# Performance work log

Hardware: AMD Instinct MI355X
Metric: run time of the kernel (lower is better)

Reference implementation:

```python
import jax, jax.numpy as jnp
import numpy as np

N_NODES = 50000
N_EDGES = 800000
DIM = 128
N_LAYERS = 4
EPS = 1e-5  # BatchNorm1d default eps


def setup_inputs() -> dict:
    key = jax.random.key(0)
    k_x, k_e, k_w = jax.random.split(key, 3)
    x = jax.random.normal(k_x, (N_NODES, DIM), dtype=jnp.float32)
    edge_index = jax.random.randint(k_e, (2, N_EDGES), 0, N_NODES, dtype=jnp.int32)
    # stacked per-layer params (input_dim == hidden_dim == DIM)
    Ws = jax.random.normal(k_w, (N_LAYERS, DIM, DIM), dtype=jnp.float32) * (1.0 / np.sqrt(DIM))
    bs = jnp.zeros((N_LAYERS, DIM), jnp.float32)
    gammas = jnp.ones((N_LAYERS, DIM), jnp.float32)
    betas = jnp.zeros((N_LAYERS, DIM), jnp.float32)
    return {"x": x, "edge_index": edge_index, "Ws": Ws, "bs": bs,
            "gammas": gammas, "betas": betas}


def gcn_conv(x, W, b, src, dst, n):
    # PyG GCNConv: h = X W; out = D^{-1/2}(A+I)D^{-1/2} h + b
    h = x @ W                                       # [N, D]
    deg = jnp.zeros((n,), h.dtype).at[dst].add(1.0) + 1.0  # +1 self-loop
    dis = jax.lax.rsqrt(deg)                        # deg > 0 due to self-loops
    msg = h[src] * (dis[src] * dis[dst])[:, None]   # [E, D] gather + scale
    out = jnp.zeros_like(h).at[dst].add(msg)        # scatter-add aggregate
    out = out + h * (dis * dis)[:, None]            # self-loop term, norm = 1/deg
    return out + b


def batchnorm(z, gamma, beta):
    # BatchNorm1d training-mode math: batch mean, biased variance
    mu = z.mean(axis=0)
    var = z.var(axis=0)
    return (z - mu) * jax.lax.rsqrt(var + EPS) * gamma + beta


def reference(x, edge_index, Ws, bs, gammas, betas):
    src, dst = edge_index[0], edge_index[1]
    z = x
    for i in range(N_LAYERS):
        z = gcn_conv(z, Ws[i], bs[i], src, dst, z.shape[0])
        z = jax.nn.relu(z)
        z = batchnorm(z, gammas[i], betas[i])
        # Dropout: identity (eval mode / deterministic reference)
    return z
```

## Files before the change

### kernel.cpp

```cpp
#include <hip/hip_runtime.h>

#define N_NODES 50000
#define N_EDGES 800000
#define DIM 128
#define NLAYERS 4
#define BN_EPS 1e-5f
#define SCAN_BLOCKS 196
#define WS2 72

typedef __attribute__((ext_vector_type(8))) short short8;
typedef __attribute__((ext_vector_type(4))) float f32x4;

__device__ __forceinline__ float bf2f(unsigned short u){
    union { unsigned int i; float f; } x; x.i = ((unsigned int)u) << 16; return x.f;
}
__device__ __forceinline__ unsigned short f2bf(float f){
    union { float f; unsigned int i; } x; x.f = f;
    unsigned int lsb = (x.i >> 16) & 1u;
    unsigned int r = x.i + 0x7fffu + lsb;
    return (unsigned short)(r >> 16);
}

struct P4 { int2 a, b, c, d; };

__device__ __forceinline__ P4 loadP_mask(const int2* __restrict__ ep, int base,
                                         int sub, int lim){
    P4 p;
    int i0 = base + sub, i1 = base + 4 + sub, i2 = base + 8 + sub, i3 = base + 12 + sub;
    p.a = (i0 < lim) ? ep[i0] : make_int2(0, 0);
    p.b = (i1 < lim) ? ep[i1] : make_int2(0, 0);
    p.c = (i2 < lim) ? ep[i2] : make_int2(0, 0);
    p.d = (i3 < lim) ? ep[i3] : make_int2(0, 0);
    return p;
}
__device__ __forceinline__ P4 loadP_full(const int2* __restrict__ ep, int base,
                                         int sub){
    P4 p;
    p.a = ep[base + sub];
    p.b = ep[base + 4 + sub];
    p.c = ep[base + 8 + sub];
    p.d = ep[base + 12 + sub];
    return p;
}
__device__ __forceinline__ P4 loadP(const int2* __restrict__ ep, int base,
                                    int sub, int lim){
    if (lim - base >= 16) return loadP_full(ep, base, sub);
    return loadP_mask(ep, base, sub, lim);
}


__global__ __launch_bounds__(256) void k_zero(int* __restrict__ p, int n){
    int i = blockIdx.x * 256 + threadIdx.x;
    if (i < n) p[i] = 0;
}

__global__ __launch_bounds__(256) void k_count(const int* __restrict__ dst,
                                               int* __restrict__ degcnt){
    int e = blockIdx.x * 256 + threadIdx.x;
    if (e < N_EDGES) atomicAdd(&degcnt[dst[e]], 1);
}

__global__ __launch_bounds__(256) void k_scan1(const int* __restrict__ degcnt,
                                               int* __restrict__ rowptr,
                                               int* __restrict__ bsum,
                                               float* __restrict__ dis){
    __shared__ int tmp[256];
    int t = threadIdx.x;
    int i = blockIdx.x * 256 + t;
    int v = (i < N_NODES) ? degcnt[i] : 0;
    if (i < N_NODES) dis[i] = rsqrtf((float)v + 1.0f);
    tmp[t] = v;
    __syncthreads();
    #pragma unroll
    for (int off = 1; off < 256; off <<= 1){
        int u = (t >= off) ? tmp[t - off] : 0;
        __syncthreads();
        tmp[t] += u;
        __syncthreads();
    }
    if (i < N_NODES) rowptr[i] = tmp[t] - v;
    if (t == 255) bsum[blockIdx.x] = tmp[255];
}

__global__ __launch_bounds__(256) void k_scan2(int* __restrict__ bsum){
    __shared__ int tmp[256];
    int t = threadIdx.x;
    int v = (t < SCAN_BLOCKS) ? bsum[t] : 0;
    tmp[t] = v;
    __syncthreads();
    #pragma unroll
    for (int off = 1; off < 256; off <<= 1){
        int u = (t >= off) ? tmp[t - off] : 0;
        __syncthreads();
        tmp[t] += u;
        __syncthreads();
    }
    if (t < SCAN_BLOCKS) bsum[t] = tmp[t] - v;
}

__global__ __launch_bounds__(256) void k_scan3(const int* __restrict__ bsum,
                                               int* __restrict__ rowptr,
                                               int* __restrict__ wptr){
    int i = blockIdx.x * 256 + threadIdx.x;
    if (i < N_NODES){
        int r = rowptr[i] + bsum[blockIdx.x];
        rowptr[i] = r; wptr[i] = r;
    }
    if (i == 0) rowptr[N_NODES] = N_EDGES;
}

__global__ __launch_bounds__(256) void k_fill(const int* __restrict__ src,
                                              const int* __restrict__ dst,
                                              const float* __restrict__ dis,
                                              int* __restrict__ wptr,
                                              int2* __restrict__ epair){
    int e = blockIdx.x * 256 + threadIdx.x;
    if (e < N_EDGES){
        int s = src[e], d = dst[e];
        float w = dis[s] * dis[d];
        int p = atomicAdd(&wptr[d], 1);
        int2 pr; pr.x = s; pr.y = __float_as_int(w);
        epair[p] = pr;
    }
}

template<bool HAS>
__global__ __launch_bounds__(256) void k_wprep(const float* __restrict__ W,
                                               const float* __restrict__ stats,
                                               const float* __restrict__ gamma,
                                               const float* __restrict__ beta,
                                               unsigned short* __restrict__ wthi,
                                               unsigned short* __restrict__ wtlo,
                                               float* __restrict__ bias2){
    int tid = threadIdx.x;
    if (blockIdx.x < 64){
        int idx = blockIdx.x * 256 + tid;
        int c = idx >> 7, k = idx & 127;
        float v = W[k*DIM + c];
        if (HAS){
            float mu  = stats[k] * (1.0f / N_NODES);
            float var = stats[DIM + k] * (1.0f / N_NODES) - mu * mu;
            float sc  = rsqrtf(var + BN_EPS) * gamma[k];
            v *= sc;
        }
        unsigned short hi = f2bf(v);
        float lo = v - bf2f(hi);
        wthi[c*DIM + k] = hi;
        wtlo[c*DIM + k] = f2bf(lo);
    } else {
        __shared__ float part[256];
        int c = tid >> 1, half = tid & 1;
        float acc = 0.f;
        if (HAS){
            int k0 = half * 64;
            #pragma unroll 4
            for (int k = k0; k < k0 + 64; k++){
                float mu  = stats[k] * (1.0f / N_NODES);
                float var = stats[DIM + k] * (1.0f / N_NODES) - mu * mu;
                float sc  = rsqrtf(var + BN_EPS) * gamma[k];
                float sh  = beta[k] - mu * sc;
                acc = fmaf(sh, W[k*DIM + c], acc);
            }
        }
        part[tid] = acc;
        __syncthreads();
        if (half == 0) bias2[c] = part[2*c] + part[2*c + 1];
    }
}


template<int MODE>
__global__ __launch_bounds__(256) void k_gemm(const void* __restrict__ zraw,
                                              const unsigned short* __restrict__ wthi,
                                              const unsigned short* __restrict__ wtlo,
                                              const float* __restrict__ bias2,
                                              unsigned short* __restrict__ hb){
    __shared__ short whi[DIM * WS2];
    __shared__ short wlo[DIM * WS2];
    int tid = threadIdx.x;

    int lane = tid & 63;
    int wv   = tid >> 6;
    int m = lane & 15;
    int q = lane >> 4;
    int row0 = blockIdx.x * 64 + wv * 16;
    int arow = row0 + m;
    bool avalid = arow < N_NODES;

    f32x4 acc[8];
    #pragma unroll
    for (int t = 0; t < 8; t++) acc[t] = (f32x4){0.f, 0.f, 0.f, 0.f};

    const uint4* gh = (const uint4*)wthi;
    const uint4* gl = (const uint4*)wtlo;

    #pragma unroll
    for (int half = 0; half < 2; half++){
        #pragma unroll
        for (int it = 0; it < 4; it++){
            int ch = tid + 256*it;
            int c = ch >> 3, k8 = ch & 7;
            int off = c*WS2 + k8*8;
            int srci = c*16 + half*8 + k8;
            *(uint4*)&whi[off] = gh[srci];
            *(uint4*)&wlo[off] = gl[srci];
        }
        __syncthreads();

        #pragma unroll
        for (int gl2 = 0; gl2 < 2; gl2++){
            int gg = half*2 + gl2;
            short8 a = {0,0,0,0,0,0,0,0};
            if (avalid){
                if (MODE == 0){
                    const float* xp = (const float*)zraw + (size_t)arow*DIM + gg*32 + q*8;
                    float4 v0 = *(const float4*)xp;
                    float4 v1 = *(const float4*)(xp + 4);
                    a[0] = (short)f2bf(v0.x); a[1] = (short)f2bf(v0.y);
                    a[2] = (short)f2bf(v0.z); a[3] = (short)f2bf(v0.w);
                    a[4] = (short)f2bf(v1.x); a[5] = (short)f2bf(v1.y);
                    a[6] = (short)f2bf(v1.z); a[7] = (short)f2bf(v1.w);
                } else {
                    a = *(const short8*)((const unsigned short*)zraw
                          + (size_t)gg*N_NODES*32 + (size_t)arow*32 + q*8);
                }
            }
            #pragma unroll
            for (int t = 0; t < 8; t++){
                int col = t*16 + m;
                int off = col*WS2 + gl2*32 + q*8;
                short8 bh = *(const short8*)&whi[off];
                short8 bl = *(const short8*)&wlo[off];
                acc[t] = __builtin_amdgcn_mfma_f32_16x16x32_bf16(a, bh, acc[t], 0, 0, 0);
                acc[t] = __builtin_amdgcn_mfma_f32_16x16x32_bf16(a, bl, acc[t], 0, 0, 0);
            }
        }
        if (half == 0) __syncthreads();
    }

    #pragma unroll
    for (int t = 0; t < 8; t++){
        int colg = t*16 + m;
        float bz = bias2[colg];
        size_t base = (size_t)(t >> 1)*N_NODES*32 + (t & 1)*16 + m;
        #pragma unroll
        for (int r = 0; r < 4; r++){
            int row = row0 + q*4 + r;
            if (row < N_NODES)
                hb[base + (size_t)row*32] = f2bf(acc[t][r] + bz);
        }
    }
}

__global__ __launch_bounds__(256) void k_agg(const unsigned short* __restrict__ h,
                                             const int* __restrict__ rowptr,
                                             const int2* __restrict__ epair,
                                             const float* __restrict__ dis,
                                             const float* __restrict__ bias,
                                             unsigned short* __restrict__ out,
                                             float* __restrict__ stats){
    int lane = threadIdx.x & 63;
    int w    = threadIdx.x >> 6;
    int g    = blockIdx.x & 3;
    int sub  = lane >> 4;
    int cp   = lane & 15;
    const ushort2* hg = (const ushort2*)(h + (size_t)g * N_NODES * 32);
    ushort2* og = (ushort2*)(out + (size_t)g * N_NODES * 32);
    float b0 = bias[g*32 + 2*cp], b1 = bias[g*32 + 2*cp + 1];
    float s0 = 0.f, s1 = 0.f, q0 = 0.f, q1 = 0.f;
    int bg = blockIdx.x >> 2;
    int nstride = (gridDim.x >> 2) * 4;

    int node = bg*4 + w;
    int ne0 = 0, ne1 = 0;
    ushort2 nhv; nhv.x = 0; nhv.y = 0;
    float ndi = 0.f;
    P4 nP = {{0,0},{0,0},{0,0},{0,0}};
    if (node < N_NODES){
        ne0 = rowptr[node];
        ne1 = rowptr[node + 1];
        nhv = hg[node*16 + cp];
        ndi = dis[node];
        nP  = loadP(epair, ne0, sub, ne1);
    }

    while (node < N_NODES){
        int e0 = ne0, e1 = ne1;
        ushort2 hv = nhv;
        float di = ndi;
        P4 P = nP;

        int nnext = node + nstride;
        if (nnext < N_NODES){
            ne0 = rowptr[nnext];
            ne1 = rowptr[nnext + 1];
            nhv = hg[nnext*16 + cp];
            ndi = dis[nnext];
        } else { ne0 = 0; ne1 = 0; }

        float pa0 = 0.f, pa1 = 0.f, pb0 = 0.f, pb1 = 0.f;
        float pc0 = 0.f, pc1 = 0.f, pd0 = 0.f, pd1 = 0.f;
        if (sub == 0){
            float dii = di * di;
            pa0 = bf2f(hv.x) * dii; pa1 = bf2f(hv.y) * dii;
        }

        int e = e0;
        while (e < e1){
            int en = e + 16;
            P4 Pn = {{0,0},{0,0},{0,0},{0,0}};
            if (en < e1) Pn = loadP(epair, en, sub, e1);
            ushort2 X0 = hg[P.a.x*16 + cp];
            ushort2 X1 = hg[P.b.x*16 + cp];
            ushort2 X2 = hg[P.c.x*16 + cp];
            ushort2 X3 = hg[P.d.x*16 + cp];
            float w0 = __int_as_float(P.a.y), w1 = __int_as_float(P.b.y);
            float w2 = __int_as_float(P.c.y), w3 = __int_as_float(P.d.y);
            pa0 = fmaf(bf2f(X0.x), w0, pa0); pa1 = fmaf(bf2f(X0.y), w0, pa1);
            pb0 = fmaf(bf2f(X1.x), w1, pb0); pb1 = fmaf(bf2f(X1.y), w1, pb1);
            pc0 = fmaf(bf2f(X2.x), w2, pc0); pc1 = fmaf(bf2f(X2.y), w2, pc1);
            pd0 = fmaf(bf2f(X3.x), w3, pd0); pd1 = fmaf(bf2f(X3.y), w3, pd1);
            P = Pn;
            e = en;
        }

        float r0 = (pa0 + pb0) + (pc0 + pd0);
        float r1 = (pa1 + pb1) + (pc1 + pd1);
        r0 += __shfl_xor(r0, 16); r1 += __shfl_xor(r1, 16);
        r0 += __shfl_xor(r0, 32); r1 += __shfl_xor(r1, 32);
        if (sub == 0){
            float a0 = fmaxf(r0 + b0, 0.f);
            float a1 = fmaxf(r1 + b1, 0.f);
            ushort2 ov; ov.x = f2bf(a0); ov.y = f2bf(a1);
            og[node*16 + cp] = ov;
            s0 += a0; s1 += a1; q0 += a0*a0; q1 += a1*a1;
        }

        if (nnext < N_NODES)
            nP = loadP(epair, ne0, sub, ne1);
        node = nnext;
    }

    __shared__ float red[4][16][4];
    if (sub == 0){
        red[w][cp][0] = s0; red[w][cp][1] = s1;
        red[w][cp][2] = q0; red[w][cp][3] = q1;
    }
    __syncthreads();
    if (w == 0 && sub == 0){
        #pragma unroll
        for (int ww = 1; ww < 4; ww++){
            s0 += red[ww][cp][0]; s1 += red[ww][cp][1];
            q0 += red[ww][cp][2]; q1 += red[ww][cp][3];
        }
        int c = g*32 + 2*cp;
        atomicAdd(&stats[c],         s0);
        atomicAdd(&stats[c + 1],     s1);
        atomicAdd(&stats[DIM + c],     q0);
        atomicAdd(&stats[DIM + c + 1], q1);
    }
}

__global__ __launch_bounds__(256) void k_bn(const uint4* __restrict__ in,
                                            const float* __restrict__ stats,
                                            const float* __restrict__ gamma,
                                            const float* __restrict__ beta,
                                            float4* __restrict__ outf){
    __shared__ float scs[DIM], shs[DIM];
    int tid = threadIdx.x;
    if (tid < DIM){
        float mu  = stats[tid] * (1.0f / N_NODES);
        float var = stats[DIM + tid] * (1.0f / N_NODES) - mu * mu;
        float sc  = rsqrtf(var + BN_EPS) * gamma[tid];
        scs[tid] = sc;
        shs[tid] = beta[tid] - mu * sc;
    }
    __syncthreads();

    int i = blockIdx.x * 256 + tid;
    if (i >= N_NODES * DIM / 8) return;
    int row = i >> 4;
    int c = (i * 8) & (DIM - 1);
    int gg = c >> 5, wi = c & 31;
    uint4 raw = in[gg*(N_NODES*4) + row*4 + (wi >> 3)];
    unsigned int u[4] = {raw.x, raw.y, raw.z, raw.w};
    float v[8];
    #pragma unroll
    for (int j = 0; j < 4; j++){
        v[2*j]   = bf2f((unsigned short)(u[j] & 0xffff));
        v[2*j+1] = bf2f((unsigned short)(u[j] >> 16));
    }
    float4 r0, r1;
    r0.x = fmaf(v[0], scs[c+0], shs[c+0]);
    r0.y = fmaf(v[1], scs[c+1], shs[c+1]);
    r0.z = fmaf(v[2], scs[c+2], shs[c+2]);
    r0.w = fmaf(v[3], scs[c+3], shs[c+3]);
    r1.x = fmaf(v[4], scs[c+4], shs[c+4]);
    r1.y = fmaf(v[5], scs[c+5], shs[c+5]);
    r1.z = fmaf(v[6], scs[c+6], shs[c+6]);
    r1.w = fmaf(v[7], scs[c+7], shs[c+7]);
    outf[2*i]   = r0;
    outf[2*i+1] = r1;
}


extern "C" void kernel_launch(void* const* d_in, const int* in_sizes, int n_in,
                              void* d_out, int out_size, void* d_ws, size_t ws_size,
                              hipStream_t stream){
    const float* x   = (const float*)d_in[0];
    const int*   src = (const int*)d_in[1];
    const int*   dst = src + N_EDGES;
    const float* Ws  = (const float*)d_in[2];
    const float* bs  = (const float*)d_in[3];
    const float* gs  = (const float*)d_in[4];
    const float* be  = (const float*)d_in[5];

    char* w = (char*)d_ws;
    int*   degcnt = (int*)(w);
    float* stats  = (float*)(w + 200000);
    float* dis    = (float*)(w + 208192);
    int*   rowptr = (int*)(w + 408192);
    int*   wptr   = (int*)(w + 608208);
    int*   bsum   = (int*)(w + 808208);
    float* bias2  = (float*)(w + 809232);
    unsigned short* wthi = (unsigned short*)(w + 809744);
    unsigned short* wtlo = (unsigned short*)(w + 842512);
    int2*  epair  = (int2*)(w + 875280);
    unsigned short* bufA = (unsigned short*)(w + 7275280);
    unsigned short* hb   = (unsigned short*)(w + 20075280);

    k_zero<<<(51024 + 255)/256, 256, 0, stream>>>(degcnt, 51024);
    k_count<<<3125, 256, 0, stream>>>(dst, degcnt);
    k_scan1<<<SCAN_BLOCKS, 256, 0, stream>>>(degcnt, rowptr, bsum, dis);
    k_scan2<<<1, 256, 0, stream>>>(bsum);
    k_scan3<<<SCAN_BLOCKS, 256, 0, stream>>>(bsum, rowptr, wptr);
    k_fill<<<3125, 256, 0, stream>>>(src, dst, dis, wptr, epair);

    for (int L = 0; L < NLAYERS; L++){
        const float* Wl = Ws + L*DIM*DIM;
        if (L == 0){
            k_wprep<false><<<65, 256, 0, stream>>>(Wl, nullptr, nullptr, nullptr,
                                                   wthi, wtlo, bias2);
            k_gemm<0><<<(N_NODES + 63)/64, 256, 0, stream>>>(x, wthi, wtlo,
                                                             bias2, hb);
        } else {
            k_wprep<true><<<65, 256, 0, stream>>>(Wl, stats + (L-1)*256,
                                                  gs + (L-1)*DIM, be + (L-1)*DIM,
                                                  wthi, wtlo, bias2);
            k_gemm<1><<<(N_NODES + 63)/64, 256, 0, stream>>>(bufA, wthi, wtlo,
                                                             bias2, hb);
        }
        k_agg<<<2048, 256, 0, stream>>>(hb, rowptr, epair, dis, bs + L*DIM,
                                        bufA, stats + L*256);
    }
    k_bn<<<3125, 256, 0, stream>>>((const uint4*)bufA, stats + 3*256,
                                   gs + 3*DIM, be + 3*DIM, (float4*)d_out);
}
```

Measured before the change: 566.1 us.

## Fuse weight prep into GEMM and merge scan kernels to cut launches

The separate weight-prep kernel, which folded the BatchNorm scale into W, split it into bf16 hi/lo parts and computed the shifted bias, is removed. Each GEMM block now does that work itself in its prologue, reading fp32 W directly. The second and third scan kernels are merged, so every block redoes the small block-sum scan locally. This drops five launches and their serialization gaps, but every one of about 782 GEMM blocks now recomputes the weight conversion with strided global reads plus a 128x128 bias reduction.

```diff
diff --git a/kernel.cpp b/kernel.cpp
--- a/kernel.cpp
+++ b/kernel.cpp
@@ -82,7 +82,9 @@
     if (t == 255) bsum[blockIdx.x] = tmp[255];
 }
 
-__global__ __launch_bounds__(256) void k_scan2(int* __restrict__ bsum){
+__global__ __launch_bounds__(256) void k_scan3(const int* __restrict__ bsum,
+                                               int* __restrict__ rowptr,
+                                               int* __restrict__ wptr){
     __shared__ int tmp[256];
     int t = threadIdx.x;
     int v = (t < SCAN_BLOCKS) ? bsum[t] : 0;
@@ -95,15 +97,10 @@
         tmp[t] += u;
         __syncthreads();
     }
-    if (t < SCAN_BLOCKS) bsum[t] = tmp[t] - v;
-}
-
-__global__ __launch_bounds__(256) void k_scan3(const int* __restrict__ bsum,
-                                               int* __restrict__ rowptr,
-                                               int* __restrict__ wptr){
-    int i = blockIdx.x * 256 + threadIdx.x;
+    int boff = (blockIdx.x == 0) ? 0 : tmp[blockIdx.x - 1];
+    int i = blockIdx.x * 256 + t;
     if (i < N_NODES){
-        int r = rowptr[i] + bsum[blockIdx.x];
+        int r = rowptr[i] + boff;
         rowptr[i] = r; wptr[i] = r;
     }
     if (i == 0) rowptr[N_NODES] = N_EDGES;
@@ -124,60 +121,42 @@
     }
 }
 
-template<bool HAS>
-__global__ __launch_bounds__(256) void k_wprep(const float* __restrict__ W,
-                                               const float* __restrict__ stats,
-                                               const float* __restrict__ gamma,
-                                               const float* __restrict__ beta,
-                                               unsigned short* __restrict__ wthi,
-                                               unsigned short* __restrict__ wtlo,
-                                               float* __restrict__ bias2){
-    int tid = threadIdx.x;
-    if (blockIdx.x < 64){
-        int idx = blockIdx.x * 256 + tid;
-        int c = idx >> 7, k = idx & 127;
-        float v = W[k*DIM + c];
-        if (HAS){
-            float mu  = stats[k] * (1.0f / N_NODES);
-            float var = stats[DIM + k] * (1.0f / N_NODES) - mu * mu;
-            float sc  = rsqrtf(var + BN_EPS) * gamma[k];
-            v *= sc;
-        }
-        unsigned short hi = f2bf(v);
-        float lo = v - bf2f(hi);
-        wthi[c*DIM + k] = hi;
-        wtlo[c*DIM + k] = f2bf(lo);
-    } else {
-        __shared__ float part[256];
-        int c = tid >> 1, half = tid & 1;
-        float acc = 0.f;
-        if (HAS){
-            int k0 = half * 64;
-            #pragma unroll 4
-            for (int k = k0; k < k0 + 64; k++){
-                float mu  = stats[k] * (1.0f / N_NODES);
-                float var = stats[DIM + k] * (1.0f / N_NODES) - mu * mu;
-                float sc  = rsqrtf(var + BN_EPS) * gamma[k];
-                float sh  = beta[k] - mu * sc;
-                acc = fmaf(sh, W[k*DIM + c], acc);
-            }
-        }
-        part[tid] = acc;
-        __syncthreads();
-        if (half == 0) bias2[c] = part[2*c] + part[2*c + 1];
-    }
-}
-
 
 template<int MODE>
 __global__ __launch_bounds__(256) void k_gemm(const void* __restrict__ zraw,
-                                              const unsigned short* __restrict__ wthi,
-                                              const unsigned short* __restrict__ wtlo,
-                                              const float* __restrict__ bias2,
+                                              const float* __restrict__ W,
+                                              const float* __restrict__ stats,
+                                              const float* __restrict__ gamma,
+                                              const float* __restrict__ beta,
                                               unsigned short* __restrict__ hb){
     __shared__ short whi[DIM * WS2];
     __shared__ short wlo[DIM * WS2];
+    __shared__ float scs[DIM], shs[DIM];
+    __shared__ float part[256];
+    __shared__ float b2[DIM];
     int tid = threadIdx.x;
+
+    if (MODE == 1){
+        if (tid < DIM){
+            float mu  = stats[tid] * (1.0f / N_NODES);
+            float var = stats[DIM + tid] * (1.0f / N_NODES) - mu * mu;
+            float sc  = rsqrtf(var + BN_EPS) * gamma[tid];
+            scs[tid] = sc;
+            shs[tid] = beta[tid] - mu * sc;
+        }
+        __syncthreads();
+        {
+            int c = tid >> 1, half = tid & 1;
+            float acc = 0.f;
+            int k0 = half * 64;
+            #pragma unroll 4
+            for (int k = k0; k < k0 + 64; k++)
+                acc = fmaf(shs[k], W[k*DIM + c], acc);
+            part[tid] = acc;
+        }
+    } else {
+        if (tid < DIM) b2[tid] = 0.f;
+    }
 
     int lane = tid & 63;
     int wv   = tid >> 6;
@@ -191,21 +170,30 @@
     #pragma unroll
     for (int t = 0; t < 8; t++) acc[t] = (f32x4){0.f, 0.f, 0.f, 0.f};
 
-    const uint4* gh = (const uint4*)wthi;
-    const uint4* gl = (const uint4*)wtlo;
-
     #pragma unroll
     for (int half = 0; half < 2; half++){
         #pragma unroll
         for (int it = 0; it < 4; it++){
             int ch = tid + 256*it;
-            int c = ch >> 3, k8 = ch & 7;
-            int off = c*WS2 + k8*8;
-            int srci = c*16 + half*8 + k8;
-            *(uint4*)&whi[off] = gh[srci];
-            *(uint4*)&wlo[off] = gl[srci];
-        }
-        __syncthreads();
+            int kc = ch >> 7, c = ch & 127;
+            int kbase = half*64 + kc*8;
+            short8 vh, vl;
+            #pragma unroll
+            for (int i = 0; i < 8; i++){
+                float v = W[(kbase + i)*DIM + c];
+                if (MODE == 1) v *= scs[kbase + i];
+                unsigned short h = f2bf(v);
+                float lo = v - bf2f(h);
+                vh[i] = (short)h;
+                vl[i] = (short)f2bf(lo);
+            }
+            *(short8*)&whi[c*WS2 + kc*8] = vh;
+            *(short8*)&wlo[c*WS2 + kc*8] = vl;
+        }
+        __syncthreads();
+        if (MODE == 1 && half == 0){
+            if (tid < DIM) b2[tid] = part[2*tid] + part[2*tid + 1];
+        }
 
         #pragma unroll
         for (int gl2 = 0; gl2 < 2; gl2++){
@@ -241,7 +229,7 @@
     #pragma unroll
     for (int t = 0; t < 8; t++){
         int colg = t*16 + m;
-        float bz = bias2[colg];
+        float bz = b2[colg];
         size_t base = (size_t)(t >> 1)*N_NODES*32 + (t & 1)*16 + m;
         #pragma unroll
         for (int r = 0; r < 4; r++){
@@ -422,9 +410,6 @@
     int*   rowptr = (int*)(w + 408192);
     int*   wptr   = (int*)(w + 608208);
     int*   bsum   = (int*)(w + 808208);
-    float* bias2  = (float*)(w + 809232);
-    unsigned short* wthi = (unsigned short*)(w + 809744);
-    unsigned short* wtlo = (unsigned short*)(w + 842512);
     int2*  epair  = (int2*)(w + 875280);
     unsigned short* bufA = (unsigned short*)(w + 7275280);
     unsigned short* hb   = (unsigned short*)(w + 20075280);
@@ -432,24 +417,17 @@
     k_zero<<<(51024 + 255)/256, 256, 0, stream>>>(degcnt, 51024);
     k_count<<<3125, 256, 0, stream>>>(dst, degcnt);
     k_scan1<<<SCAN_BLOCKS, 256, 0, stream>>>(degcnt, rowptr, bsum, dis);
-    k_scan2<<<1, 256, 0, stream>>>(bsum);
     k_scan3<<<SCAN_BLOCKS, 256, 0, stream>>>(bsum, rowptr, wptr);
     k_fill<<<3125, 256, 0, stream>>>(src, dst, dis, wptr, epair);
 
     for (int L = 0; L < NLAYERS; L++){
         const float* Wl = Ws + L*DIM*DIM;
-        if (L == 0){
-            k_wprep<false><<<65, 256, 0, stream>>>(Wl, nullptr, nullptr, nullptr,
-                                                   wthi, wtlo, bias2);
-            k_gemm<0><<<(N_NODES + 63)/64, 256, 0, stream>>>(x, wthi, wtlo,
-                                                             bias2, hb);
-        } else {
-            k_wprep<true><<<65, 256, 0, stream>>>(Wl, stats + (L-1)*256,
-                                                  gs + (L-1)*DIM, be + (L-1)*DIM,
-                                                  wthi, wtlo, bias2);
-            k_gemm<1><<<(N_NODES + 63)/64, 256, 0, stream>>>(bufA, wthi, wtlo,
-                                                             bias2, hb);
-        }
+        if (L == 0)
+            k_gemm<0><<<(N_NODES + 63)/64, 256, 0, stream>>>(x, Wl,
+                    nullptr, nullptr, nullptr, hb);
+        else
+            k_gemm<1><<<(N_NODES + 63)/64, 256, 0, stream>>>(bufA, Wl,
+                    stats + (L-1)*256, gs + (L-1)*DIM, be + (L-1)*DIM, hb);
         k_agg<<<2048, 256, 0, stream>>>(hb, rowptr, epair, dis, bs + L*DIM,
                                         bufA, stats + L*256);
     }
```

New measurement: 552.8 us. 1.02x faster.
